# Performance work log

Measured on AMD Instinct MI355X. Metric: run time of the kernel, lower is better.

Reference implementation:

```python
import jax, jax.numpy as jnp
import numpy as np

N, E = 30000, 480000
IN_C, HID, HEADS = 128, 32, 8
HC = HID * HEADS  # 256
EPS = 1e-5
NEG_SLOPE = 0.2


def setup_inputs() -> dict:
    key = jax.random.key(0)
    ks = jax.random.split(key, 20)
    s = 0.05
    return {
        "x": jax.random.normal(ks[0], (N, IN_C), jnp.float32),
        "edge_index": jax.random.randint(ks[1], (2, E), 0, N, jnp.int32),
        "W1": jax.random.normal(ks[2], (IN_C, HC), jnp.float32) * s,
        "a1_src": jax.random.normal(ks[3], (HEADS, HID), jnp.float32) * s,
        "a1_dst": jax.random.normal(ks[4], (HEADS, HID), jnp.float32) * s,
        "b1": jnp.zeros((HC,), jnp.float32),
        "g1": jnp.ones((HC,), jnp.float32),
        "be1": jnp.zeros((HC,), jnp.float32),
        "W2": jax.random.normal(ks[5], (HC, HC), jnp.float32) * s,
        "a2_src": jax.random.normal(ks[6], (HEADS, HID), jnp.float32) * s,
        "a2_dst": jax.random.normal(ks[7], (HEADS, HID), jnp.float32) * s,
        "b2": jnp.zeros((HC,), jnp.float32),
        "g2": jnp.ones((HC,), jnp.float32),
        "be2": jnp.zeros((HC,), jnp.float32),
        "lW1": jax.random.normal(ks[8], (HC, HID), jnp.float32) * s,
        "lb1": jnp.zeros((HID,), jnp.float32),
        "lW2": jax.random.normal(ks[9], (HID, 1), jnp.float32) * s,
        "lb2": jnp.zeros((1,), jnp.float32),
    }


def gat_layer(x, src, dst, W, a_s, a_d, b):
    # x: [N, Fin] -> h: [N, H, C]
    h = (x @ W).reshape(N, HEADS, HID)
    al_s = jnp.sum(h * a_s, axis=-1)  # [N, H]
    al_d = jnp.sum(h * a_d, axis=-1)  # [N, H]
    e = jax.nn.leaky_relu(al_s[src] + al_d[dst], NEG_SLOPE)  # [E', H]
    # segment softmax over incoming edges of each destination node
    e = e - jax.ops.segment_max(e, dst, num_segments=N)[dst]
    ex = jnp.exp(e)
    alpha = ex / jax.ops.segment_sum(ex, dst, num_segments=N)[dst]
    msg = h[src] * alpha[:, :, None]  # [E', H, C]
    out = jax.ops.segment_sum(msg, dst, num_segments=N)  # [N, H, C]
    return out.reshape(N, HC) + b


def batchnorm(x, g, b):
    m = jnp.mean(x, axis=0)
    v = jnp.var(x, axis=0)
    return (x - m) * jax.lax.rsqrt(v + EPS) * g + b


def reference(x, edge_index, W1, a1_src, a1_dst, b1, g1, be1,
              W2, a2_src, a2_dst, b2, g2, be2, lW1, lb1, lW2, lb2):
    # add self-loops (PyG GATConv default)
    loop = jnp.arange(N, dtype=edge_index.dtype)
    src = jnp.concatenate([edge_index[0], loop])
    dst = jnp.concatenate([edge_index[1], loop])

    h = jax.nn.elu(gat_layer(x, src, dst, W1, a1_src, a1_dst, b1))
    h = batchnorm(h, g1, be1)
    h = jax.nn.elu(gat_layer(h, src, dst, W2, a2_src, a2_dst, b2))
    h = batchnorm(h, g2, be2)
    h = jax.nn.elu(h @ lW1 + lb1)
    return h @ lW2 + lb2
```

## Files before the change

### kernel.cpp

```cpp
#include <hip/hip_runtime.h>
#include <math.h>

#define N_NODES 30000
#define E_EDGES 480000
#define EP (E_EDGES + N_NODES)
#define IN_CH 128
#define HID 32
#define HEADS 8
#define HC 256
#define BN_EPS 1e-5f
#define NEG_SLOPE 0.2f
#define SCAN_NB ((N_NODES + 1023) / 1024)
#define PART_SLOTS 64

typedef __attribute__((ext_vector_type(8))) short bf16x8;
typedef __attribute__((ext_vector_type(4))) float f32x4;

__device__ __forceinline__ float elu_f(float x) { return x > 0.f ? x : __expf(x) - 1.f; }
__device__ __forceinline__ float lrelu_f(float x) { return x >= 0.f ? x : NEG_SLOPE * x; }
__device__ __forceinline__ float bf2f(unsigned short u) {
    return __uint_as_float(((unsigned)u) << 16);
}
__device__ __forceinline__ unsigned short f2bf(float f) {
    unsigned u = __float_as_uint(f);
    return (unsigned short)((u + 0x7fffu + ((u >> 16) & 1u)) >> 16);
}

__global__ void wt_all_kernel(const float* __restrict__ W1, const float* __restrict__ W2,
                              const float* __restrict__ lW1,
                              unsigned short* __restrict__ wt1,
                              unsigned short* __restrict__ wt2,
                              unsigned short* __restrict__ wtm) {
    int i = blockIdx.x * 256 + threadIdx.x;
    if (i < IN_CH * HC) {
        int k = i >> 8, n = i & 255;
        wt1[(size_t)n * IN_CH + k] = f2bf(W1[i]);
    } else if (i < IN_CH * HC + HC * HC) {
        int j = i - IN_CH * HC;
        int k = j >> 8, n = j & 255;
        wt2[(size_t)n * HC + k] = f2bf(W2[j]);
    } else if (i < IN_CH * HC + HC * HC + HC * HID) {
        int j = i - IN_CH * HC - HC * HC;
        int k = j >> 5, n = j & 31;
        wtm[(size_t)n * HC + k] = f2bf(lW1[j]);
    }
}

__global__ __launch_bounds__(256) void gemm_mfma(const float* __restrict__ A32,
                                                 const unsigned short* __restrict__ Abf,
                                                 const unsigned short* __restrict__ Bt,
                                                 unsigned short* __restrict__ C,
                                                 float* __restrict__ al_s,
                                                 float* __restrict__ al_d,
                                                 const float* __restrict__ a_src,
                                                 const float* __restrict__ a_dst,
                                                 int M, int K,
                                                 const float* __restrict__ sc,
                                                 const float* __restrict__ sh) {
    __shared__ __align__(16) unsigned short As[64][40];
    __shared__ __align__(16) unsigned short Bs[256][40];
    int tid = threadIdx.x;
    int wave = tid >> 6, lane = tid & 63;
    int m = lane & 15, q = lane >> 4;
    int row0 = blockIdx.x * 64;
    f32x4 acc[4][4];
#pragma unroll
    for (int i = 0; i < 4; ++i)
#pragma unroll
        for (int j = 0; j < 4; ++j) acc[i][j] = (f32x4){0.f, 0.f, 0.f, 0.f};
    int ar = tid >> 2, aseg = tid & 3;
    for (int k0 = 0; k0 < K; k0 += 32) {
        float4 v0 = make_float4(0.f, 0.f, 0.f, 0.f), v1 = v0;
        int gr = row0 + ar;
        int c0 = k0 + aseg * 8;
        if (gr < M) {
            if (A32) {
                const float* ap = A32 + (size_t)gr * K + c0;
                v0 = *(const float4*)ap;
                v1 = *(const float4*)(ap + 4);
            } else {
                uint4 raw = *(const uint4*)(Abf + (size_t)gr * K + c0);
                v0.x = bf2f((unsigned short)raw.x); v0.y = bf2f((unsigned short)(raw.x >> 16));
                v0.z = bf2f((unsigned short)raw.y); v0.w = bf2f((unsigned short)(raw.y >> 16));
                v1.x = bf2f((unsigned short)raw.z); v1.y = bf2f((unsigned short)(raw.z >> 16));
                v1.z = bf2f((unsigned short)raw.w); v1.w = bf2f((unsigned short)(raw.w >> 16));
            }
        }
        if (sc) {
            float4 s0 = *(const float4*)(sc + c0), s1 = *(const float4*)(sc + c0 + 4);
            float4 t0 = *(const float4*)(sh + c0), t1 = *(const float4*)(sh + c0 + 4);
            v0.x = v0.x * s0.x + t0.x; v0.y = v0.y * s0.y + t0.y;
            v0.z = v0.z * s0.z + t0.z; v0.w = v0.w * s0.w + t0.w;
            v1.x = v1.x * s1.x + t1.x; v1.y = v1.y * s1.y + t1.y;
            v1.z = v1.z * s1.z + t1.z; v1.w = v1.w * s1.w + t1.w;
        }
        bf16x8 av;
        av[0] = (short)f2bf(v0.x); av[1] = (short)f2bf(v0.y);
        av[2] = (short)f2bf(v0.z); av[3] = (short)f2bf(v0.w);
        av[4] = (short)f2bf(v1.x); av[5] = (short)f2bf(v1.y);
        av[6] = (short)f2bf(v1.z); av[7] = (short)f2bf(v1.w);
        *(bf16x8*)(&As[ar][aseg * 8]) = av;
        const unsigned short* bp = Bt + (size_t)tid * K + k0;
#pragma unroll
        for (int sg = 0; sg < 4; ++sg)
            *(uint4*)(&Bs[tid][sg * 8]) = *(const uint4*)(bp + sg * 8);
        __syncthreads();
        bf16x8 a0 = *(const bf16x8*)(&As[m][q * 8]);
        bf16x8 a1 = *(const bf16x8*)(&As[16 + m][q * 8]);
        bf16x8 a2 = *(const bf16x8*)(&As[32 + m][q * 8]);
        bf16x8 a3 = *(const bf16x8*)(&As[48 + m][q * 8]);
#pragma unroll
        for (int ni = 0; ni < 4; ++ni) {
            bf16x8 b = *(const bf16x8*)(&Bs[(wave * 4 + ni) * 16 + m][q * 8]);
            acc[0][ni] = __builtin_amdgcn_mfma_f32_16x16x32_bf16(a0, b, acc[0][ni], 0, 0, 0);
            acc[1][ni] = __builtin_amdgcn_mfma_f32_16x16x32_bf16(a1, b, acc[1][ni], 0, 0, 0);
            acc[2][ni] = __builtin_amdgcn_mfma_f32_16x16x32_bf16(a2, b, acc[2][ni], 0, 0, 0);
            acc[3][ni] = __builtin_amdgcn_mfma_f32_16x16x32_bf16(a3, b, acc[3][ni], 0, 0, 0);
        }
        __syncthreads();
    }
    int col0 = wave * 64;
    float asv[4], adv[4];
#pragma unroll
    for (int ni = 0; ni < 4; ++ni) {
        asv[ni] = a_src[col0 + ni * 16 + m];
        adv[ni] = a_dst[col0 + ni * 16 + m];
    }
#pragma unroll
    for (int mi = 0; mi < 4; ++mi) {
#pragma unroll
        for (int r = 0; r < 4; ++r) {
            int grow = row0 + mi * 16 + q * 4 + r;
            bool gv = grow < M;
            if (gv) {
#pragma unroll
                for (int ni = 0; ni < 4; ++ni)
                    C[(size_t)grow * HC + col0 + ni * 16 + m] = f2bf(acc[mi][ni][r]);
            }
            float ps0 = acc[mi][0][r] * asv[0] + acc[mi][1][r] * asv[1];
            float pd0 = acc[mi][0][r] * adv[0] + acc[mi][1][r] * adv[1];
            float ps1 = acc[mi][2][r] * asv[2] + acc[mi][3][r] * asv[3];
            float pd1 = acc[mi][2][r] * adv[2] + acc[mi][3][r] * adv[3];
            ps0 += __shfl_xor(ps0, 1); pd0 += __shfl_xor(pd0, 1);
            ps1 += __shfl_xor(ps1, 1); pd1 += __shfl_xor(pd1, 1);
            ps0 += __shfl_xor(ps0, 2); pd0 += __shfl_xor(pd0, 2);
            ps1 += __shfl_xor(ps1, 2); pd1 += __shfl_xor(pd1, 2);
            ps0 += __shfl_xor(ps0, 4); pd0 += __shfl_xor(pd0, 4);
            ps1 += __shfl_xor(ps1, 4); pd1 += __shfl_xor(pd1, 4);
            ps0 += __shfl_xor(ps0, 8); pd0 += __shfl_xor(pd0, 8);
            ps1 += __shfl_xor(ps1, 8); pd1 += __shfl_xor(pd1, 8);
            if (gv) {
                if (m == 0) {
                    al_s[grow * HEADS + 2 * wave] = ps0;
                    al_d[grow * HEADS + 2 * wave] = pd0;
                } else if (m == 1) {
                    al_s[grow * HEADS + 2 * wave + 1] = ps1;
                    al_d[grow * HEADS + 2 * wave + 1] = pd1;
                }
            }
        }
    }
}

__global__ void deg_kernel(const int* __restrict__ ei, int* __restrict__ deg,
                           float* __restrict__ part) {
    int e = blockIdx.x * blockDim.x + threadIdx.x;
    if (e < 2 * PART_SLOTS * 512) part[e] = 0.f;
    if (e >= EP) return;
    int d = (e < E_EDGES) ? ei[E_EDGES + e] : e - E_EDGES;
    atomicAdd(deg + d, 1);
}

__global__ __launch_bounds__(1024) void scan_blk(const int* __restrict__ deg,
                                                 int* __restrict__ rs,
                                                 int* __restrict__ bsum) {
    __shared__ int sh[1024];
    int t = threadIdx.x;
    int i = blockIdx.x * 1024 + t;
    int v = (i < N_NODES) ? deg[i] : 0;
    sh[t] = v;
    __syncthreads();
    for (int off = 1; off < 1024; off <<= 1) {
        int tv = (t >= off) ? sh[t - off] : 0;
        __syncthreads();
        sh[t] += tv;
        __syncthreads();
    }
    if (i < N_NODES) rs[i] = sh[t] - v;
    if (t == 1023) bsum[blockIdx.x] = sh[1023];
}

__global__ __launch_bounds__(1024) void scan_add(int* __restrict__ rs,
                                                 int* __restrict__ cursor,
                                                 const int* __restrict__ bsum) {
    __shared__ int sh_off, sh_tot;
    int t = threadIdx.x;
    if (t < 64) {
        int v = (t < SCAN_NB) ? bsum[t] : 0;
        int pre = (t < (int)blockIdx.x) ? v : 0;
        int tot = v;
#pragma unroll
        for (int off = 1; off < 64; off <<= 1) {
            tot += __shfl_xor(tot, off);
            pre += __shfl_xor(pre, off);
        }
        if (t == 0) { sh_off = pre; sh_tot = tot; }
    }
    __syncthreads();
    int i = blockIdx.x * 1024 + t;
    if (i < N_NODES) {
        int v = rs[i] + sh_off;
        rs[i] = v;
        cursor[i] = v;
    } else if (i == N_NODES) {
        rs[N_NODES] = sh_tot;
    }
}

__global__ void scatter_kernel(const int* __restrict__ ei, int* __restrict__ cursor,
                               int* __restrict__ csr_src) {
    int e = blockIdx.x * blockDim.x + threadIdx.x;
    if (e >= EP) return;
    int s, d;
    if (e < E_EDGES) { s = ei[e]; d = ei[E_EDGES + e]; } else { s = d = e - E_EDGES; }
    int pos = atomicAdd(cursor + d, 1);
    csr_src[pos] = s;
}

__global__ __launch_bounds__(256) void attn_kernel(const uint4* __restrict__ h8,
                                                   const float* __restrict__ al_s,
                                                   const float* __restrict__ al_d,
                                                   const int* __restrict__ row_start,
                                                   const int* __restrict__ csr_src,
                                                   const float4* __restrict__ bias4,
                                                   uint4* __restrict__ out8,
                                                   float* __restrict__ part) {
    __shared__ float lds_s[4][256];
    __shared__ float lds_q[4][256];
    int wave = threadIdx.x >> 6;
    int d = blockIdx.x * 4 + wave;
    int lane = threadIdx.x & 63;
    int hh = lane & 7, eo = lane >> 3;
    int g = lane >> 5, c = lane & 31;
    int hl = c >> 2;
    int beg = row_start[d], end = row_start[d + 1];
    float ad = al_d[d * HEADS + hh];
    float ssum = 0.f;
    float acc[8];
#pragma unroll
    for (int t = 0; t < 8; ++t) acc[t] = 0.f;

#define PAIR_BODY(p)                                                      \
    {                                                                     \
        int e0 = 2 * (p) + g;                                             \
        int sj = __shfl(sreg, e0 * 8);                                    \
        float aj = __shfl(ex, e0 * 8 + hl);                               \
        uint4 v = h8[(size_t)sj * 32 + c];                                \
        acc[0] += aj * bf2f((unsigned short)v.x);                         \
        acc[1] += aj * bf2f((unsigned short)(v.x >> 16));                 \
        acc[2] += aj * bf2f((unsigned short)v.y);                         \
        acc[3] += aj * bf2f((unsigned short)(v.y >> 16));                 \
        acc[4] += aj * bf2f((unsigned short)v.z);                         \
        acc[5] += aj * bf2f((unsigned short)(v.z >> 16));                 \
        acc[6] += aj * bf2f((unsigned short)v.w);                         \
        acc[7] += aj * bf2f((unsigned short)(v.w >> 16));                 \
    }

    for (int i = beg; i < end; i += 8) {
        int chunk = end - i;
        if (chunk > 8) chunk = 8;
        int sreg = 0;
        float ex = 0.f;
        if (eo < chunk) {
            sreg = csr_src[i + eo];
            ex = __expf(lrelu_f(al_s[sreg * HEADS + hh] + ad));
        }
        ssum += ex;
        if (chunk == 8) {
#pragma unroll
            for (int p = 0; p < 4; ++p) PAIR_BODY(p);
        } else {
            int np = (chunk + 1) >> 1;
            for (int p = 0; p < np; ++p) PAIR_BODY(p);
        }
    }
#undef PAIR_BODY

#pragma unroll
    for (int t = 0; t < 8; ++t) acc[t] += __shfl_xor(acc[t], 32);
    ssum += __shfl_xor(ssum, 8);
    ssum += __shfl_xor(ssum, 16);
    ssum += __shfl_xor(ssum, 32);
    float inv = 1.f / __shfl(ssum, hl);

    float4 b0 = bias4[c * 2], b1 = bias4[c * 2 + 1];
    float o0 = elu_f(acc[0] * inv + b0.x);
    float o1 = elu_f(acc[1] * inv + b0.y);
    float o2 = elu_f(acc[2] * inv + b0.z);
    float o3 = elu_f(acc[3] * inv + b0.w);
    float o4 = elu_f(acc[4] * inv + b1.x);
    float o5 = elu_f(acc[5] * inv + b1.y);
    float o6 = elu_f(acc[6] * inv + b1.z);
    float o7 = elu_f(acc[7] * inv + b1.w);

    if (g == 0) {
        uint4 ov;
        ov.x = (unsigned)f2bf(o0) | ((unsigned)f2bf(o1) << 16);
        ov.y = (unsigned)f2bf(o2) | ((unsigned)f2bf(o3) << 16);
        ov.z = (unsigned)f2bf(o4) | ((unsigned)f2bf(o5) << 16);
        ov.w = (unsigned)f2bf(o6) | ((unsigned)f2bf(o7) << 16);
        out8[(size_t)d * 32 + c] = ov;
        int cb = c * 8;
        lds_s[wave][cb + 0] = o0; lds_q[wave][cb + 0] = o0 * o0;
        lds_s[wave][cb + 1] = o1; lds_q[wave][cb + 1] = o1 * o1;
        lds_s[wave][cb + 2] = o2; lds_q[wave][cb + 2] = o2 * o2;
        lds_s[wave][cb + 3] = o3; lds_q[wave][cb + 3] = o3 * o3;
        lds_s[wave][cb + 4] = o4; lds_q[wave][cb + 4] = o4 * o4;
        lds_s[wave][cb + 5] = o5; lds_q[wave][cb + 5] = o5 * o5;
        lds_s[wave][cb + 6] = o6; lds_q[wave][cb + 6] = o6 * o6;
        lds_s[wave][cb + 7] = o7; lds_q[wave][cb + 7] = o7 * o7;
    }
    __syncthreads();
    int ch = threadIdx.x;
    float s = lds_s[0][ch] + lds_s[1][ch] + lds_s[2][ch] + lds_s[3][ch];
    float q = lds_q[0][ch] + lds_q[1][ch] + lds_q[2][ch] + lds_q[3][ch];
    float* pb = part + (size_t)(blockIdx.x & (PART_SLOTS - 1)) * 512;
    atomicAdd(pb + ch, s);
    atomicAdd(pb + 256 + ch, q);
}

__global__ void bn_fin_kernel(const float* __restrict__ part,
                              const float* __restrict__ g, const float* __restrict__ be,
                              float* __restrict__ scale, float* __restrict__ shift) {
    int c = threadIdx.x;
    float s = 0.f, q = 0.f;
#pragma unroll
    for (int b = 0; b < PART_SLOTS; ++b) {
        s += part[(size_t)b * 512 + c];
        q += part[(size_t)b * 512 + 256 + c];
    }
    float m = s / (float)N_NODES;
    float var = q / (float)N_NODES - m * m;
    float istd = rsqrtf(var + BN_EPS);
    float sc = istd * g[c];
    scale[c] = sc;
    shift[c] = be[c] - m * sc;
}

__global__ __launch_bounds__(256) void mlp_mfma(const unsigned short* __restrict__ in,
                                                const float* __restrict__ sc,
                                                const float* __restrict__ sh,
                                                const unsigned short* __restrict__ Wt,
                                                const float* __restrict__ lb1,
                                                const float* __restrict__ lW2,
                                                const float* __restrict__ lb2,
                                                float* __restrict__ out) {
    int tid = threadIdx.x;
    int wave = tid >> 6, lane = tid & 63;
    int m = lane & 15, q = lane >> 4;
    int rbase = blockIdx.x * 64 + wave * 16;
    int arow = rbase + m;
    bool valid = arow < N_NODES;
    const unsigned short* ap = in + (size_t)arow * HC;
    f32x4 acc0 = (f32x4){0.f, 0.f, 0.f, 0.f}, acc1 = acc0;
#pragma unroll
    for (int k0 = 0; k0 < HC; k0 += 32) {
        int c0 = k0 + q * 8;
        bf16x8 b0 = *(const bf16x8*)(Wt + (size_t)m * HC + c0);
        bf16x8 b1 = *(const bf16x8*)(Wt + (size_t)(m + 16) * HC + c0);
        bf16x8 a = (bf16x8){0, 0, 0, 0, 0, 0, 0, 0};
        if (valid) {
            uint4 raw = *(const uint4*)(ap + c0);
            float v0 = bf2f((unsigned short)raw.x), v1 = bf2f((unsigned short)(raw.x >> 16));
            float v2 = bf2f((unsigned short)raw.y), v3 = bf2f((unsigned short)(raw.y >> 16));
            float v4 = bf2f((unsigned short)raw.z), v5 = bf2f((unsigned short)(raw.z >> 16));
            float v6 = bf2f((unsigned short)raw.w), v7 = bf2f((unsigned short)(raw.w >> 16));
            float4 s0 = *(const float4*)(sc + c0), s1 = *(const float4*)(sc + c0 + 4);
            float4 t0 = *(const float4*)(sh + c0), t1 = *(const float4*)(sh + c0 + 4);
            a[0] = (short)f2bf(v0 * s0.x + t0.x);
            a[1] = (short)f2bf(v1 * s0.y + t0.y);
            a[2] = (short)f2bf(v2 * s0.z + t0.z);
            a[3] = (short)f2bf(v3 * s0.w + t0.w);
            a[4] = (short)f2bf(v4 * s1.x + t1.x);
            a[5] = (short)f2bf(v5 * s1.y + t1.y);
            a[6] = (short)f2bf(v6 * s1.z + t1.z);
            a[7] = (short)f2bf(v7 * s1.w + t1.w);
        }
        acc0 = __builtin_amdgcn_mfma_f32_16x16x32_bf16(a, b0, acc0, 0, 0, 0);
        acc1 = __builtin_amdgcn_mfma_f32_16x16x32_bf16(a, b1, acc1, 0, 0, 0);
    }
    float w2a = lW2[m], w2b = lW2[m + 16];
    float ba = lb1[m], bb = lb1[m + 16];
#pragma unroll
    for (int r = 0; r < 4; ++r) {
        float v = elu_f(acc0[r] + ba) * w2a + elu_f(acc1[r] + bb) * w2b;
        v += __shfl_xor(v, 1);
        v += __shfl_xor(v, 2);
        v += __shfl_xor(v, 4);
        v += __shfl_xor(v, 8);
        int orow = rbase + q * 4 + r;
        if (m == 0 && orow < N_NODES) out[orow] = v + lb2[0];
    }
}

extern "C" void kernel_launch(void* const* d_in, const int* in_sizes, int n_in,
                              void* d_out, int out_size, void* d_ws, size_t ws_size,
                              hipStream_t stream) {
    const float* x   = (const float*)d_in[0];
    const int*   ei  = (const int*)d_in[1];
    const float* W1  = (const float*)d_in[2];
    const float* a1s = (const float*)d_in[3];
    const float* a1d = (const float*)d_in[4];
    const float* b1  = (const float*)d_in[5];
    const float* g1  = (const float*)d_in[6];
    const float* be1 = (const float*)d_in[7];
    const float* W2  = (const float*)d_in[8];
    const float* a2s = (const float*)d_in[9];
    const float* a2d = (const float*)d_in[10];
    const float* b2  = (const float*)d_in[11];
    const float* g2  = (const float*)d_in[12];
    const float* be2 = (const float*)d_in[13];
    const float* lW1 = (const float*)d_in[14];
    const float* lb1 = (const float*)d_in[15];
    const float* lW2 = (const float*)d_in[16];
    const float* lb2 = (const float*)d_in[17];
    float* out = (float*)d_out;

    char* p = (char*)d_ws;
    auto alloc = [&](size_t bytes) {
        char* r = p;
        p += (bytes + 255) & ~(size_t)255;
        return r;
    };
    unsigned short* h_bf  = (unsigned short*)alloc((size_t)N_NODES * HC * 2);
    unsigned short* o_bf  = (unsigned short*)alloc((size_t)N_NODES * HC * 2);
    unsigned short* wt1   = (unsigned short*)alloc((size_t)IN_CH * HC * 2);
    unsigned short* wt2   = (unsigned short*)alloc((size_t)HC * HC * 2);
    unsigned short* wtm   = (unsigned short*)alloc((size_t)HC * HID * 2);
    float* f_als  = (float*)alloc((size_t)N_NODES * HEADS * 4);
    float* f_ald  = (float*)alloc((size_t)N_NODES * HEADS * 4);
    int*   i_deg  = (int*)alloc((size_t)N_NODES * 4);
    int*   i_rs   = (int*)alloc((size_t)(N_NODES + 1) * 4);
    int*   i_cur  = (int*)alloc((size_t)N_NODES * 4);
    int*   i_src  = (int*)alloc((size_t)EP * 4);
    int*   i_bsum = (int*)alloc((size_t)(SCAN_NB + 1) * 4);
    float* f_part = (float*)alloc((size_t)2 * PART_SLOTS * 512 * 4);
    float* f_sc1  = (float*)alloc(HC * 4);
    float* f_sh1  = (float*)alloc(HC * 4);
    float* f_sc2  = (float*)alloc(HC * 4);
    float* f_sh2  = (float*)alloc(HC * 4);

    int eb = (EP + 255) / 256;

    hipMemsetAsync(i_deg, 0, (size_t)N_NODES * 4, stream);
    deg_kernel<<<eb, 256, 0, stream>>>(ei, i_deg, f_part);
    scan_blk<<<SCAN_NB, 1024, 0, stream>>>(i_deg, i_rs, i_bsum);
    scan_add<<<SCAN_NB, 1024, 0, stream>>>(i_rs, i_cur, i_bsum);
    scatter_kernel<<<eb, 256, 0, stream>>>(ei, i_cur, i_src);

    int wtot = IN_CH * HC + HC * HC + HC * HID;
    wt_all_kernel<<<(wtot + 255) / 256, 256, 0, stream>>>(W1, W2, lW1, wt1, wt2, wtm);

    int gblocks = (N_NODES + 63) / 64;

    auto run_layer = [&](const float* A32, const unsigned short* Abf, int K,
                         const unsigned short* wt, const float* in_sc, const float* in_sh,
                         const float* as_, const float* ad_, const float* bias,
                         const float* gam, const float* bet, float* part,
                         float* out_sc, float* out_sh) {
        gemm_mfma<<<gblocks, 256, 0, stream>>>(A32, Abf, wt, h_bf, f_als, f_ald, as_, ad_,
                                               N_NODES, K, in_sc, in_sh);
        attn_kernel<<<N_NODES / 4, 256, 0, stream>>>((const uint4*)h_bf, f_als, f_ald,
                                                     i_rs, i_src, (const float4*)bias,
                                                     (uint4*)o_bf, part);
        bn_fin_kernel<<<1, 256, 0, stream>>>(part, gam, bet, out_sc, out_sh);
    };

    run_layer(x, nullptr, IN_CH, wt1, nullptr, nullptr, a1s, a1d, b1, g1, be1,
              f_part, f_sc1, f_sh1);
    run_layer(nullptr, o_bf, HC, wt2, f_sc1, f_sh1, a2s, a2d, b2, g2, be2,
              f_part + (size_t)PART_SLOTS * 512, f_sc2, f_sh2);

    mlp_mfma<<<gblocks, 256, 0, stream>>>(o_bf, f_sc2, f_sh2, wtm, lb1, lW2, lb2, out);
}
```

Before: 295.6 us.

## Fold BN finalize into consumers, enlarge GEMM tile, batch attention gathers

Removes the separate single-block BN finalize kernels; each GEMM and MLP block now reduces the partial sums itself into shared scale/shift. The GEMM block grows to 512 threads covering 128 rows, so each B tile staged in shared memory is reused by twice as many rows. The attention loop handles 16 edges per iteration and issues all eight row gathers before the FMAs, to keep more memory loads in flight. The cost is that every block repeats the 64-slot partial reduction, and the larger unrolled loop uses more registers.

```diff
diff --git a/kernel.cpp b/kernel.cpp
--- a/kernel.cpp
+++ b/kernel.cpp
@@ -46,7 +46,7 @@
     }
 }
 
-__global__ __launch_bounds__(256) void gemm_mfma(const float* __restrict__ A32,
+__global__ __launch_bounds__(512) void gemm_mfma(const float* __restrict__ A32,
                                                  const unsigned short* __restrict__ Abf,
                                                  const unsigned short* __restrict__ Bt,
                                                  unsigned short* __restrict__ C,
@@ -55,20 +55,44 @@
                                                  const float* __restrict__ a_src,
                                                  const float* __restrict__ a_dst,
                                                  int M, int K,
-                                                 const float* __restrict__ sc,
-                                                 const float* __restrict__ sh) {
-    __shared__ __align__(16) unsigned short As[64][40];
+                                                 const float* __restrict__ part,
+                                                 const float* __restrict__ gam,
+                                                 const float* __restrict__ bet) {
+    __shared__ __align__(16) unsigned short As[128][40];
     __shared__ __align__(16) unsigned short Bs[256][40];
+    __shared__ float scs[HC], shs[HC];
     int tid = threadIdx.x;
     int wave = tid >> 6, lane = tid & 63;
     int m = lane & 15, q = lane >> 4;
-    int row0 = blockIdx.x * 64;
+    int wr = (wave >> 2) * 64;
+    int hp = wave & 3;
+    int col0 = hp * 64;
+    int row0 = blockIdx.x * 128;
+    bool haveBN = (part != nullptr);
+    if (haveBN && tid < HC) {
+        int c = tid;
+        float s = 0.f, qq = 0.f;
+#pragma unroll
+        for (int b = 0; b < PART_SLOTS; ++b) {
+            s += part[(size_t)b * 512 + c];
+            qq += part[(size_t)b * 512 + 256 + c];
+        }
+        float mn = s / (float)N_NODES;
+        float var = qq / (float)N_NODES - mn * mn;
+        float istd = rsqrtf(var + BN_EPS);
+        float sc = istd * gam[c];
+        scs[c] = sc;
+        shs[c] = bet[c] - mn * sc;
+    }
+    __syncthreads();
+
     f32x4 acc[4][4];
 #pragma unroll
     for (int i = 0; i < 4; ++i)
 #pragma unroll
         for (int j = 0; j < 4; ++j) acc[i][j] = (f32x4){0.f, 0.f, 0.f, 0.f};
     int ar = tid >> 2, aseg = tid & 3;
+    int br = tid >> 1, bseg = tid & 1;
     for (int k0 = 0; k0 < K; k0 += 32) {
         float4 v0 = make_float4(0.f, 0.f, 0.f, 0.f), v1 = v0;
         int gr = row0 + ar;
@@ -86,9 +110,9 @@
                 v1.z = bf2f((unsigned short)raw.w); v1.w = bf2f((unsigned short)(raw.w >> 16));
             }
         }
-        if (sc) {
-            float4 s0 = *(const float4*)(sc + c0), s1 = *(const float4*)(sc + c0 + 4);
-            float4 t0 = *(const float4*)(sh + c0), t1 = *(const float4*)(sh + c0 + 4);
+        if (haveBN) {
+            float4 s0 = *(const float4*)(scs + c0), s1 = *(const float4*)(scs + c0 + 4);
+            float4 t0 = *(const float4*)(shs + c0), t1 = *(const float4*)(shs + c0 + 4);
             v0.x = v0.x * s0.x + t0.x; v0.y = v0.y * s0.y + t0.y;
             v0.z = v0.z * s0.z + t0.z; v0.w = v0.w * s0.w + t0.w;
             v1.x = v1.x * s1.x + t1.x; v1.y = v1.y * s1.y + t1.y;
@@ -100,18 +124,17 @@
         av[4] = (short)f2bf(v1.x); av[5] = (short)f2bf(v1.y);
         av[6] = (short)f2bf(v1.z); av[7] = (short)f2bf(v1.w);
         *(bf16x8*)(&As[ar][aseg * 8]) = av;
-        const unsigned short* bp = Bt + (size_t)tid * K + k0;
-#pragma unroll
-        for (int sg = 0; sg < 4; ++sg)
-            *(uint4*)(&Bs[tid][sg * 8]) = *(const uint4*)(bp + sg * 8);
+        const unsigned short* bp = Bt + (size_t)br * K + k0 + bseg * 16;
+        *(uint4*)(&Bs[br][bseg * 16]) = *(const uint4*)bp;
+        *(uint4*)(&Bs[br][bseg * 16 + 8]) = *(const uint4*)(bp + 8);
         __syncthreads();
-        bf16x8 a0 = *(const bf16x8*)(&As[m][q * 8]);
-        bf16x8 a1 = *(const bf16x8*)(&As[16 + m][q * 8]);
-        bf16x8 a2 = *(const bf16x8*)(&As[32 + m][q * 8]);
-        bf16x8 a3 = *(const bf16x8*)(&As[48 + m][q * 8]);
+        bf16x8 a0 = *(const bf16x8*)(&As[wr + m][q * 8]);
+        bf16x8 a1 = *(const bf16x8*)(&As[wr + 16 + m][q * 8]);
+        bf16x8 a2 = *(const bf16x8*)(&As[wr + 32 + m][q * 8]);
+        bf16x8 a3 = *(const bf16x8*)(&As[wr + 48 + m][q * 8]);
 #pragma unroll
         for (int ni = 0; ni < 4; ++ni) {
-            bf16x8 b = *(const bf16x8*)(&Bs[(wave * 4 + ni) * 16 + m][q * 8]);
+            bf16x8 b = *(const bf16x8*)(&Bs[col0 + ni * 16 + m][q * 8]);
             acc[0][ni] = __builtin_amdgcn_mfma_f32_16x16x32_bf16(a0, b, acc[0][ni], 0, 0, 0);
             acc[1][ni] = __builtin_amdgcn_mfma_f32_16x16x32_bf16(a1, b, acc[1][ni], 0, 0, 0);
             acc[2][ni] = __builtin_amdgcn_mfma_f32_16x16x32_bf16(a2, b, acc[2][ni], 0, 0, 0);
@@ -119,7 +142,6 @@
         }
         __syncthreads();
     }
-    int col0 = wave * 64;
     float asv[4], adv[4];
 #pragma unroll
     for (int ni = 0; ni < 4; ++ni) {
@@ -130,7 +152,7 @@
     for (int mi = 0; mi < 4; ++mi) {
 #pragma unroll
         for (int r = 0; r < 4; ++r) {
-            int grow = row0 + mi * 16 + q * 4 + r;
+            int grow = row0 + wr + mi * 16 + q * 4 + r;
             bool gv = grow < M;
             if (gv) {
 #pragma unroll
@@ -151,11 +173,11 @@
             ps1 += __shfl_xor(ps1, 8); pd1 += __shfl_xor(pd1, 8);
             if (gv) {
                 if (m == 0) {
-                    al_s[grow * HEADS + 2 * wave] = ps0;
-                    al_d[grow * HEADS + 2 * wave] = pd0;
+                    al_s[grow * HEADS + 2 * hp] = ps0;
+                    al_d[grow * HEADS + 2 * hp] = pd0;
                 } else if (m == 1) {
-                    al_s[grow * HEADS + 2 * wave + 1] = ps1;
-                    al_d[grow * HEADS + 2 * wave + 1] = pd1;
+                    al_s[grow * HEADS + 2 * hp + 1] = ps1;
+                    al_d[grow * HEADS + 2 * hp + 1] = pd1;
                 }
             }
         }
@@ -250,12 +272,8 @@
 #pragma unroll
     for (int t = 0; t < 8; ++t) acc[t] = 0.f;
 
-#define PAIR_BODY(p)                                                      \
+#define FMA8(v, aj)                                                       \
     {                                                                     \
-        int e0 = 2 * (p) + g;                                             \
-        int sj = __shfl(sreg, e0 * 8);                                    \
-        float aj = __shfl(ex, e0 * 8 + hl);                               \
-        uint4 v = h8[(size_t)sj * 32 + c];                                \
         acc[0] += aj * bf2f((unsigned short)v.x);                         \
         acc[1] += aj * bf2f((unsigned short)(v.x >> 16));                 \
         acc[2] += aj * bf2f((unsigned short)v.y);                         \
@@ -265,26 +283,49 @@
         acc[6] += aj * bf2f((unsigned short)v.w);                         \
         acc[7] += aj * bf2f((unsigned short)(v.w >> 16));                 \
     }
-
-    for (int i = beg; i < end; i += 8) {
-        int chunk = end - i;
-        if (chunk > 8) chunk = 8;
-        int sreg = 0;
-        float ex = 0.f;
-        if (eo < chunk) {
-            sreg = csr_src[i + eo];
-            ex = __expf(lrelu_f(al_s[sreg * HEADS + hh] + ad));
-        }
-        ssum += ex;
-        if (chunk == 8) {
-#pragma unroll
-            for (int p = 0; p < 4; ++p) PAIR_BODY(p);
+#define PRE(k, SR, EX, p)                                                 \
+    int sj##k = __shfl(SR, (2 * (p) + g) * 8);                            \
+    float aj##k = __shfl(EX, (2 * (p) + g) * 8 + hl);                     \
+    uint4 w##k = h8[(size_t)sj##k * 32 + c];
+#define PAIR(SR, EX, p)                                                   \
+    {                                                                     \
+        PRE(t, SR, EX, p)                                                 \
+        FMA8(w##t, aj##t)                                                 \
+    }
+
+    for (int i = beg; i < end; i += 16) {
+        int rem = end - i;
+        int cntA = rem > 8 ? 8 : rem;
+        int cntB = rem > 8 ? (rem > 16 ? 8 : rem - 8) : 0;
+        int sregA = 0, sregB = 0;
+        float exA = 0.f, exB = 0.f;
+        if (eo < cntA) {
+            sregA = csr_src[i + eo];
+            exA = __expf(lrelu_f(al_s[sregA * HEADS + hh] + ad));
+        }
+        if (eo < cntB) {
+            sregB = csr_src[i + 8 + eo];
+            exB = __expf(lrelu_f(al_s[sregB * HEADS + hh] + ad));
+        }
+        ssum += exA;
+        ssum += exB;
+        if (rem >= 16) {
+            PRE(0, sregA, exA, 0) PRE(1, sregA, exA, 1)
+            PRE(2, sregA, exA, 2) PRE(3, sregA, exA, 3)
+            PRE(4, sregB, exB, 0) PRE(5, sregB, exB, 1)
+            PRE(6, sregB, exB, 2) PRE(7, sregB, exB, 3)
+            FMA8(w0, aj0) FMA8(w1, aj1) FMA8(w2, aj2) FMA8(w3, aj3)
+            FMA8(w4, aj4) FMA8(w5, aj5) FMA8(w6, aj6) FMA8(w7, aj7)
         } else {
-            int np = (chunk + 1) >> 1;
-            for (int p = 0; p < np; ++p) PAIR_BODY(p);
-        }
-    }
-#undef PAIR_BODY
+            int npA = (cntA + 1) >> 1;
+            for (int p = 0; p < npA; ++p) PAIR(sregA, exA, p);
+            int npB = (cntB + 1) >> 1;
+            for (int p = 0; p < npB; ++p) PAIR(sregB, exB, p);
+        }
+    }
+#undef PAIR
+#undef PRE
+#undef FMA8
 
 #pragma unroll
     for (int t = 0; t < 8; ++t) acc[t] += __shfl_xor(acc[t], 32);
@@ -329,33 +370,33 @@
     atomicAdd(pb + 256 + ch, q);
 }
 
-__global__ void bn_fin_kernel(const float* __restrict__ part,
-                              const float* __restrict__ g, const float* __restrict__ be,
-                              float* __restrict__ scale, float* __restrict__ shift) {
-    int c = threadIdx.x;
-    float s = 0.f, q = 0.f;
-#pragma unroll
-    for (int b = 0; b < PART_SLOTS; ++b) {
-        s += part[(size_t)b * 512 + c];
-        q += part[(size_t)b * 512 + 256 + c];
-    }
-    float m = s / (float)N_NODES;
-    float var = q / (float)N_NODES - m * m;
-    float istd = rsqrtf(var + BN_EPS);
-    float sc = istd * g[c];
-    scale[c] = sc;
-    shift[c] = be[c] - m * sc;
-}
-
 __global__ __launch_bounds__(256) void mlp_mfma(const unsigned short* __restrict__ in,
-                                                const float* __restrict__ sc,
-                                                const float* __restrict__ sh,
+                                                const float* __restrict__ part,
+                                                const float* __restrict__ gam,
+                                                const float* __restrict__ bet,
                                                 const unsigned short* __restrict__ Wt,
                                                 const float* __restrict__ lb1,
                                                 const float* __restrict__ lW2,
                                                 const float* __restrict__ lb2,
                                                 float* __restrict__ out) {
+    __shared__ float scs[HC], shs[HC];
     int tid = threadIdx.x;
+    {
+        int c = tid;
+        float s = 0.f, qq = 0.f;
+#pragma unroll
+        for (int b = 0; b < PART_SLOTS; ++b) {
+            s += part[(size_t)b * 512 + c];
+            qq += part[(size_t)b * 512 + 256 + c];
+        }
+        float mn = s / (float)N_NODES;
+        float var = qq / (float)N_NODES - mn * mn;
+        float istd = rsqrtf(var + BN_EPS);
+        float sc = istd * gam[c];
+        scs[c] = sc;
+        shs[c] = bet[c] - mn * sc;
+    }
+    __syncthreads();
     int wave = tid >> 6, lane = tid & 63;
     int m = lane & 15, q = lane >> 4;
     int rbase = blockIdx.x * 64 + wave * 16;
@@ -375,8 +416,8 @@
             float v2 = bf2f((unsigned short)raw.y), v3 = bf2f((unsigned short)(raw.y >> 16));
             float v4 = bf2f((unsigned short)raw.z), v5 = bf2f((unsigned short)(raw.z >> 16));
             float v6 = bf2f((unsigned short)raw.w), v7 = bf2f((unsigned short)(raw.w >> 16));
-            float4 s0 = *(const float4*)(sc + c0), s1 = *(const float4*)(sc + c0 + 4);
-            float4 t0 = *(const float4*)(sh + c0), t1 = *(const float4*)(sh + c0 + 4);
+            float4 s0 = *(const float4*)(scs + c0), s1 = *(const float4*)(scs + c0 + 4);
+            float4 t0 = *(const float4*)(shs + c0), t1 = *(const float4*)(shs + c0 + 4);
             a[0] = (short)f2bf(v0 * s0.x + t0.x);
             a[1] = (short)f2bf(v1 * s0.y + t0.y);
             a[2] = (short)f2bf(v2 * s0.z + t0.z);
@@ -445,10 +486,6 @@
     int*   i_src  = (int*)alloc((size_t)EP * 4);
     int*   i_bsum = (int*)alloc((size_t)(SCAN_NB + 1) * 4);
     float* f_part = (float*)alloc((size_t)2 * PART_SLOTS * 512 * 4);
-    float* f_sc1  = (float*)alloc(HC * 4);
-    float* f_sh1  = (float*)alloc(HC * 4);
-    float* f_sc2  = (float*)alloc(HC * 4);
-    float* f_sh2  = (float*)alloc(HC * 4);
 
     int eb = (EP + 255) / 256;
 
@@ -461,25 +498,20 @@
     int wtot = IN_CH * HC + HC * HC + HC * HID;
     wt_all_kernel<<<(wtot + 255) / 256, 256, 0, stream>>>(W1, W2, lW1, wt1, wt2, wtm);
 
-    int gblocks = (N_NODES + 63) / 64;
-
-    auto run_layer = [&](const float* A32, const unsigned short* Abf, int K,
-                         const unsigned short* wt, const float* in_sc, const float* in_sh,
-                         const float* as_, const float* ad_, const float* bias,
-                         const float* gam, const float* bet, float* part,
-                         float* out_sc, float* out_sh) {
-        gemm_mfma<<<gblocks, 256, 0, stream>>>(A32, Abf, wt, h_bf, f_als, f_ald, as_, ad_,
-                                               N_NODES, K, in_sc, in_sh);
-        attn_kernel<<<N_NODES / 4, 256, 0, stream>>>((const uint4*)h_bf, f_als, f_ald,
-                                                     i_rs, i_src, (const float4*)bias,
-                                                     (uint4*)o_bf, part);
-        bn_fin_kernel<<<1, 256, 0, stream>>>(part, gam, bet, out_sc, out_sh);
-    };
-
-    run_layer(x, nullptr, IN_CH, wt1, nullptr, nullptr, a1s, a1d, b1, g1, be1,
-              f_part, f_sc1, f_sh1);
-    run_layer(nullptr, o_bf, HC, wt2, f_sc1, f_sh1, a2s, a2d, b2, g2, be2,
-              f_part + (size_t)PART_SLOTS * 512, f_sc2, f_sh2);
-
-    mlp_mfma<<<gblocks, 256, 0, stream>>>(o_bf, f_sc2, f_sh2, wtm, lb1, lW2, lb2, out);
-}
+    int gblocks = (N_NODES + 127) / 128;
+    float* part1 = f_part;
+    float* part2 = f_part + (size_t)PART_SLOTS * 512;
+
+    gemm_mfma<<<gblocks, 512, 0, stream>>>(x, nullptr, wt1, h_bf, f_als, f_ald, a1s, a1d,
+                                           N_NODES, IN_CH, nullptr, nullptr, nullptr);
+    attn_kernel<<<N_NODES / 4, 256, 0, stream>>>((const uint4*)h_bf, f_als, f_ald,
+                                                 i_rs, i_src, (const float4*)b1,
+                                                 (uint4*)o_bf, part1);
+    gemm_mfma<<<gblocks, 512, 0, stream>>>(nullptr, o_bf, wt2, h_bf, f_als, f_ald, a2s, a2d,
+                                           N_NODES, HC, part1, g1, be1);
+    attn_kernel<<<N_NODES / 4, 256, 0, stream>>>((const uint4*)h_bf, f_als, f_ald,
+                                                 i_rs, i_src, (const float4*)b2,
+                                                 (uint4*)o_bf, part2);
+    mlp_mfma<<<(N_NODES + 63) / 64, 256, 0, stream>>>(o_bf, part2, g2, be2, wtm,
+                                                      lb1, lW2, lb2, out);
+}
```

Result: no change. 295.3 us (-0.1%).

## Fold batchnorm into next-layer weights and use async LDS loads in GEMM

Applied to the files above, without the earlier changes.

Batchnorm scale and shift are folded into the following weight matrices and a per-column bias (fold2/fold3 kernels), so the GEMM and MLP read plain bf16 activations without per-element affine transforms. The GEMM now stages tiles with global_load_lds into a swizzled LDS layout and uses 128-row tiles with 512 threads. The input x is converted to bf16 by a separate pass. Folding the scale into the weights before bf16 rounding changes rounding behaviour slightly. The GEMM has no row bounds check on its loads and instead relies on padded input buffers (M_PAD).

```diff
diff --git a/kernel.cpp b/kernel.cpp
--- a/kernel.cpp
+++ b/kernel.cpp
@@ -12,6 +12,7 @@
 #define NEG_SLOPE 0.2f
 #define SCAN_NB ((N_NODES + 1023) / 1024)
 #define PART_SLOTS 64
+#define M_PAD 30080
 
 typedef __attribute__((ext_vector_type(8))) short bf16x8;
 typedef __attribute__((ext_vector_type(4))) float f32x4;
@@ -26,92 +27,148 @@
     return (unsigned short)((u + 0x7fffu + ((u >> 16) & 1u)) >> 16);
 }
 
-__global__ void wt_all_kernel(const float* __restrict__ W1, const float* __restrict__ W2,
-                              const float* __restrict__ lW1,
-                              unsigned short* __restrict__ wt1,
-                              unsigned short* __restrict__ wt2,
-                              unsigned short* __restrict__ wtm) {
+#define GLD16(gp, lp)                                                      \
+    __builtin_amdgcn_global_load_lds(                                      \
+        (const __attribute__((address_space(1))) unsigned int*)(gp),       \
+        (__attribute__((address_space(3))) unsigned int*)(lp), 16, 0, 0)
+
+__global__ void wt_all_kernel(const float* __restrict__ W1,
+                              unsigned short* __restrict__ wt1) {
     int i = blockIdx.x * 256 + threadIdx.x;
     if (i < IN_CH * HC) {
         int k = i >> 8, n = i & 255;
         wt1[(size_t)n * IN_CH + k] = f2bf(W1[i]);
-    } else if (i < IN_CH * HC + HC * HC) {
-        int j = i - IN_CH * HC;
-        int k = j >> 8, n = j & 255;
-        wt2[(size_t)n * HC + k] = f2bf(W2[j]);
-    } else if (i < IN_CH * HC + HC * HC + HC * HID) {
-        int j = i - IN_CH * HC - HC * HC;
-        int k = j >> 5, n = j & 31;
-        wtm[(size_t)n * HC + k] = f2bf(lW1[j]);
-    }
-}
-
-__global__ __launch_bounds__(256) void gemm_mfma(const float* __restrict__ A32,
-                                                 const unsigned short* __restrict__ Abf,
+    }
+}
+
+__global__ void xconv_kernel(const float* __restrict__ x, unsigned short* __restrict__ xbf) {
+    int i = blockIdx.x * 256 + threadIdx.x;
+    if (i * 8 >= N_NODES * IN_CH) return;
+    const float4* xp = (const float4*)(x + (size_t)i * 8);
+    float4 v0 = xp[0], v1 = xp[1];
+    ushort4 o0, o1;
+    o0.x = f2bf(v0.x); o0.y = f2bf(v0.y); o0.z = f2bf(v0.z); o0.w = f2bf(v0.w);
+    o1.x = f2bf(v1.x); o1.y = f2bf(v1.y); o1.z = f2bf(v1.z); o1.w = f2bf(v1.w);
+    ushort4* op = (ushort4*)(xbf + (size_t)i * 8);
+    op[0] = o0; op[1] = o1;
+}
+
+__global__ __launch_bounds__(256) void fold2_kernel(const float* __restrict__ W2,
+                                                    const float* __restrict__ part,
+                                                    const float* __restrict__ g,
+                                                    const float* __restrict__ be,
+                                                    unsigned short* __restrict__ wt2p,
+                                                    float* __restrict__ cb2) {
+    __shared__ float red[256];
+    int n = blockIdx.x, k = threadIdx.x;
+    float s = 0.f, qq = 0.f;
+#pragma unroll
+    for (int b = 0; b < PART_SLOTS; ++b) {
+        s += part[(size_t)b * 512 + k];
+        qq += part[(size_t)b * 512 + 256 + k];
+    }
+    float mn = s / (float)N_NODES;
+    float var = qq / (float)N_NODES - mn * mn;
+    float istd = rsqrtf(var + BN_EPS);
+    float sck = istd * g[k];
+    float shk = be[k] - mn * sck;
+    float w = W2[(size_t)k * HC + n];
+    wt2p[(size_t)n * HC + k] = f2bf(w * sck);
+    red[k] = shk * w;
+    __syncthreads();
+    for (int off = 128; off > 0; off >>= 1) {
+        if (k < off) red[k] += red[k + off];
+        __syncthreads();
+    }
+    if (k == 0) cb2[n] = red[0];
+}
+
+__global__ __launch_bounds__(256) void fold3_kernel(const float* __restrict__ lW1,
+                                                    const float* __restrict__ part,
+                                                    const float* __restrict__ g,
+                                                    const float* __restrict__ be,
+                                                    const float* __restrict__ lb1,
+                                                    unsigned short* __restrict__ wtmp,
+                                                    float* __restrict__ lb1p) {
+    __shared__ float red[256];
+    int n = blockIdx.x, k = threadIdx.x;
+    float s = 0.f, qq = 0.f;
+#pragma unroll
+    for (int b = 0; b < PART_SLOTS; ++b) {
+        s += part[(size_t)b * 512 + k];
+        qq += part[(size_t)b * 512 + 256 + k];
+    }
+    float mn = s / (float)N_NODES;
+    float var = qq / (float)N_NODES - mn * mn;
+    float istd = rsqrtf(var + BN_EPS);
+    float sck = istd * g[k];
+    float shk = be[k] - mn * sck;
+    float w = lW1[(size_t)k * HID + n];
+    wtmp[(size_t)n * HC + k] = f2bf(w * sck);
+    red[k] = shk * w;
+    __syncthreads();
+    for (int off = 128; off > 0; off >>= 1) {
+        if (k < off) red[k] += red[k + off];
+        __syncthreads();
+    }
+    if (k == 0) lb1p[n] = lb1[n] + red[0];
+}
+
+__global__ __launch_bounds__(512) void gemm_mfma(const unsigned short* __restrict__ Abf,
                                                  const unsigned short* __restrict__ Bt,
+                                                 const float* __restrict__ cb,
                                                  unsigned short* __restrict__ C,
                                                  float* __restrict__ al_s,
                                                  float* __restrict__ al_d,
                                                  const float* __restrict__ a_src,
                                                  const float* __restrict__ a_dst,
-                                                 int M, int K,
-                                                 const float* __restrict__ sc,
-                                                 const float* __restrict__ sh) {
-    __shared__ __align__(16) unsigned short As[64][40];
-    __shared__ __align__(16) unsigned short Bs[256][40];
+                                                 int M, int K) {
+    __shared__ __align__(16) unsigned short As[128 * 32];
+    __shared__ __align__(16) unsigned short Bs[256 * 32];
     int tid = threadIdx.x;
     int wave = tid >> 6, lane = tid & 63;
     int m = lane & 15, q = lane >> 4;
-    int row0 = blockIdx.x * 64;
+    int wr = (wave >> 2) * 64;
+    int hp = wave & 3;
+    int col0 = hp * 64;
+    int row0 = blockIdx.x * 128;
+
+    int sA = wave * 64 + lane;
+    int rA = sA >> 2, scA = sA & 3;
+    int ccA = scA ^ (rA & 3) ^ ((rA >> 2) & 3);
+    const unsigned short* aSrc = Abf + (size_t)(row0 + rA) * K + ccA * 8;
+    unsigned short* aDst = As + wave * 512;
+    int sB0 = wave * 128 + lane;
+    int rB0 = sB0 >> 2, scB0 = sB0 & 3;
+    int ccB0 = scB0 ^ (rB0 & 3) ^ ((rB0 >> 2) & 3);
+    const unsigned short* bSrc0 = Bt + (size_t)rB0 * K + ccB0 * 8;
+    unsigned short* bDst0 = Bs + wave * 1024;
+    int sB1 = sB0 + 64;
+    int rB1 = sB1 >> 2, scB1 = sB1 & 3;
+    int ccB1 = scB1 ^ (rB1 & 3) ^ ((rB1 >> 2) & 3);
+    const unsigned short* bSrc1 = Bt + (size_t)rB1 * K + ccB1 * 8;
+    unsigned short* bDst1 = Bs + wave * 1024 + 512;
+
+    int ccr8 = (q ^ (m & 3) ^ ((m >> 2) & 3)) * 8;
+
     f32x4 acc[4][4];
 #pragma unroll
     for (int i = 0; i < 4; ++i)
 #pragma unroll
         for (int j = 0; j < 4; ++j) acc[i][j] = (f32x4){0.f, 0.f, 0.f, 0.f};
-    int ar = tid >> 2, aseg = tid & 3;
+
     for (int k0 = 0; k0 < K; k0 += 32) {
-        float4 v0 = make_float4(0.f, 0.f, 0.f, 0.f), v1 = v0;
-        int gr = row0 + ar;
-        int c0 = k0 + aseg * 8;
-        if (gr < M) {
-            if (A32) {
-                const float* ap = A32 + (size_t)gr * K + c0;
-                v0 = *(const float4*)ap;
-                v1 = *(const float4*)(ap + 4);
-            } else {
-                uint4 raw = *(const uint4*)(Abf + (size_t)gr * K + c0);
-                v0.x = bf2f((unsigned short)raw.x); v0.y = bf2f((unsigned short)(raw.x >> 16));
-                v0.z = bf2f((unsigned short)raw.y); v0.w = bf2f((unsigned short)(raw.y >> 16));
-                v1.x = bf2f((unsigned short)raw.z); v1.y = bf2f((unsigned short)(raw.z >> 16));
-                v1.z = bf2f((unsigned short)raw.w); v1.w = bf2f((unsigned short)(raw.w >> 16));
-            }
-        }
-        if (sc) {
-            float4 s0 = *(const float4*)(sc + c0), s1 = *(const float4*)(sc + c0 + 4);
-            float4 t0 = *(const float4*)(sh + c0), t1 = *(const float4*)(sh + c0 + 4);
-            v0.x = v0.x * s0.x + t0.x; v0.y = v0.y * s0.y + t0.y;
-            v0.z = v0.z * s0.z + t0.z; v0.w = v0.w * s0.w + t0.w;
-            v1.x = v1.x * s1.x + t1.x; v1.y = v1.y * s1.y + t1.y;
-            v1.z = v1.z * s1.z + t1.z; v1.w = v1.w * s1.w + t1.w;
-        }
-        bf16x8 av;
-        av[0] = (short)f2bf(v0.x); av[1] = (short)f2bf(v0.y);
-        av[2] = (short)f2bf(v0.z); av[3] = (short)f2bf(v0.w);
-        av[4] = (short)f2bf(v1.x); av[5] = (short)f2bf(v1.y);
-        av[6] = (short)f2bf(v1.z); av[7] = (short)f2bf(v1.w);
-        *(bf16x8*)(&As[ar][aseg * 8]) = av;
-        const unsigned short* bp = Bt + (size_t)tid * K + k0;
-#pragma unroll
-        for (int sg = 0; sg < 4; ++sg)
-            *(uint4*)(&Bs[tid][sg * 8]) = *(const uint4*)(bp + sg * 8);
+        GLD16(aSrc + k0, aDst);
+        GLD16(bSrc0 + k0, bDst0);
+        GLD16(bSrc1 + k0, bDst1);
         __syncthreads();
-        bf16x8 a0 = *(const bf16x8*)(&As[m][q * 8]);
-        bf16x8 a1 = *(const bf16x8*)(&As[16 + m][q * 8]);
-        bf16x8 a2 = *(const bf16x8*)(&As[32 + m][q * 8]);
-        bf16x8 a3 = *(const bf16x8*)(&As[48 + m][q * 8]);
+        bf16x8 a0 = *(const bf16x8*)(As + (wr + m) * 32 + ccr8);
+        bf16x8 a1 = *(const bf16x8*)(As + (wr + 16 + m) * 32 + ccr8);
+        bf16x8 a2 = *(const bf16x8*)(As + (wr + 32 + m) * 32 + ccr8);
+        bf16x8 a3 = *(const bf16x8*)(As + (wr + 48 + m) * 32 + ccr8);
 #pragma unroll
         for (int ni = 0; ni < 4; ++ni) {
-            bf16x8 b = *(const bf16x8*)(&Bs[(wave * 4 + ni) * 16 + m][q * 8]);
+            bf16x8 b = *(const bf16x8*)(Bs + (col0 + ni * 16 + m) * 32 + ccr8);
             acc[0][ni] = __builtin_amdgcn_mfma_f32_16x16x32_bf16(a0, b, acc[0][ni], 0, 0, 0);
             acc[1][ni] = __builtin_amdgcn_mfma_f32_16x16x32_bf16(a1, b, acc[1][ni], 0, 0, 0);
             acc[2][ni] = __builtin_amdgcn_mfma_f32_16x16x32_bf16(a2, b, acc[2][ni], 0, 0, 0);
@@ -119,7 +176,16 @@
         }
         __syncthreads();
     }
-    int col0 = wave * 64;
+    float cbv[4];
+#pragma unroll
+    for (int ni = 0; ni < 4; ++ni) cbv[ni] = cb[col0 + ni * 16 + m];
+#pragma unroll
+    for (int mi = 0; mi < 4; ++mi)
+#pragma unroll
+        for (int ni = 0; ni < 4; ++ni)
+#pragma unroll
+            for (int r = 0; r < 4; ++r) acc[mi][ni][r] += cbv[ni];
+
     float asv[4], adv[4];
 #pragma unroll
     for (int ni = 0; ni < 4; ++ni) {
@@ -130,7 +196,7 @@
     for (int mi = 0; mi < 4; ++mi) {
 #pragma unroll
         for (int r = 0; r < 4; ++r) {
-            int grow = row0 + mi * 16 + q * 4 + r;
+            int grow = row0 + wr + mi * 16 + q * 4 + r;
             bool gv = grow < M;
             if (gv) {
 #pragma unroll
@@ -151,11 +217,11 @@
             ps1 += __shfl_xor(ps1, 8); pd1 += __shfl_xor(pd1, 8);
             if (gv) {
                 if (m == 0) {
-                    al_s[grow * HEADS + 2 * wave] = ps0;
-                    al_d[grow * HEADS + 2 * wave] = pd0;
+                    al_s[grow * HEADS + 2 * hp] = ps0;
+                    al_d[grow * HEADS + 2 * hp] = pd0;
                 } else if (m == 1) {
-                    al_s[grow * HEADS + 2 * wave + 1] = ps1;
-                    al_d[grow * HEADS + 2 * wave + 1] = pd1;
+                    al_s[grow * HEADS + 2 * hp + 1] = ps1;
+                    al_d[grow * HEADS + 2 * hp + 1] = pd1;
                 }
             }
         }
@@ -165,7 +231,7 @@
 __global__ void deg_kernel(const int* __restrict__ ei, int* __restrict__ deg,
                            float* __restrict__ part) {
     int e = blockIdx.x * blockDim.x + threadIdx.x;
-    if (e < 2 * PART_SLOTS * 512) part[e] = 0.f;
+    if (e < 2 * PART_SLOTS * 512 + 256) part[e] = 0.f;
     if (e >= EP) return;
     int d = (e < E_EDGES) ? ei[E_EDGES + e] : e - E_EDGES;
     atomicAdd(deg + d, 1);
@@ -329,29 +395,9 @@
     atomicAdd(pb + 256 + ch, q);
 }
 
-__global__ void bn_fin_kernel(const float* __restrict__ part,
-                              const float* __restrict__ g, const float* __restrict__ be,
-                              float* __restrict__ scale, float* __restrict__ shift) {
-    int c = threadIdx.x;
-    float s = 0.f, q = 0.f;
-#pragma unroll
-    for (int b = 0; b < PART_SLOTS; ++b) {
-        s += part[(size_t)b * 512 + c];
-        q += part[(size_t)b * 512 + 256 + c];
-    }
-    float m = s / (float)N_NODES;
-    float var = q / (float)N_NODES - m * m;
-    float istd = rsqrtf(var + BN_EPS);
-    float sc = istd * g[c];
-    scale[c] = sc;
-    shift[c] = be[c] - m * sc;
-}
-
 __global__ __launch_bounds__(256) void mlp_mfma(const unsigned short* __restrict__ in,
-                                                const float* __restrict__ sc,
-                                                const float* __restrict__ sh,
                                                 const unsigned short* __restrict__ Wt,
-                                                const float* __restrict__ lb1,
+                                                const float* __restrict__ lb1p,
                                                 const float* __restrict__ lW2,
                                                 const float* __restrict__ lb2,
                                                 float* __restrict__ out) {
@@ -369,28 +415,12 @@
         bf16x8 b0 = *(const bf16x8*)(Wt + (size_t)m * HC + c0);
         bf16x8 b1 = *(const bf16x8*)(Wt + (size_t)(m + 16) * HC + c0);
         bf16x8 a = (bf16x8){0, 0, 0, 0, 0, 0, 0, 0};
-        if (valid) {
-            uint4 raw = *(const uint4*)(ap + c0);
-            float v0 = bf2f((unsigned short)raw.x), v1 = bf2f((unsigned short)(raw.x >> 16));
-            float v2 = bf2f((unsigned short)raw.y), v3 = bf2f((unsigned short)(raw.y >> 16));
-            float v4 = bf2f((unsigned short)raw.z), v5 = bf2f((unsigned short)(raw.z >> 16));
-            float v6 = bf2f((unsigned short)raw.w), v7 = bf2f((unsigned short)(raw.w >> 16));
-            float4 s0 = *(const float4*)(sc + c0), s1 = *(const float4*)(sc + c0 + 4);
-            float4 t0 = *(const float4*)(sh + c0), t1 = *(const float4*)(sh + c0 + 4);
-            a[0] = (short)f2bf(v0 * s0.x + t0.x);
-            a[1] = (short)f2bf(v1 * s0.y + t0.y);
-            a[2] = (short)f2bf(v2 * s0.z + t0.z);
-            a[3] = (short)f2bf(v3 * s0.w + t0.w);
-            a[4] = (short)f2bf(v4 * s1.x + t1.x);
-            a[5] = (short)f2bf(v5 * s1.y + t1.y);
-            a[6] = (short)f2bf(v6 * s1.z + t1.z);
-            a[7] = (short)f2bf(v7 * s1.w + t1.w);
-        }
+        if (valid) a = *(const bf16x8*)(ap + c0);
         acc0 = __builtin_amdgcn_mfma_f32_16x16x32_bf16(a, b0, acc0, 0, 0, 0);
         acc1 = __builtin_amdgcn_mfma_f32_16x16x32_bf16(a, b1, acc1, 0, 0, 0);
     }
     float w2a = lW2[m], w2b = lW2[m + 16];
-    float ba = lb1[m], bb = lb1[m + 16];
+    float ba = lb1p[m], bb = lb1p[m + 16];
 #pragma unroll
     for (int r = 0; r < 4; ++r) {
         float v = elu_f(acc0[r] + ba) * w2a + elu_f(acc1[r] + bb) * w2b;
@@ -432,11 +462,12 @@
         p += (bytes + 255) & ~(size_t)255;
         return r;
     };
+    unsigned short* x_bf  = (unsigned short*)alloc((size_t)M_PAD * IN_CH * 2);
     unsigned short* h_bf  = (unsigned short*)alloc((size_t)N_NODES * HC * 2);
-    unsigned short* o_bf  = (unsigned short*)alloc((size_t)N_NODES * HC * 2);
+    unsigned short* o_bf  = (unsigned short*)alloc((size_t)M_PAD * HC * 2);
     unsigned short* wt1   = (unsigned short*)alloc((size_t)IN_CH * HC * 2);
-    unsigned short* wt2   = (unsigned short*)alloc((size_t)HC * HC * 2);
-    unsigned short* wtm   = (unsigned short*)alloc((size_t)HC * HID * 2);
+    unsigned short* wt2p  = (unsigned short*)alloc((size_t)HC * HC * 2);
+    unsigned short* wtmp  = (unsigned short*)alloc((size_t)HC * HID * 2);
     float* f_als  = (float*)alloc((size_t)N_NODES * HEADS * 4);
     float* f_ald  = (float*)alloc((size_t)N_NODES * HEADS * 4);
     int*   i_deg  = (int*)alloc((size_t)N_NODES * 4);
@@ -444,11 +475,13 @@
     int*   i_cur  = (int*)alloc((size_t)N_NODES * 4);
     int*   i_src  = (int*)alloc((size_t)EP * 4);
     int*   i_bsum = (int*)alloc((size_t)(SCAN_NB + 1) * 4);
-    float* f_part = (float*)alloc((size_t)2 * PART_SLOTS * 512 * 4);
-    float* f_sc1  = (float*)alloc(HC * 4);
-    float* f_sh1  = (float*)alloc(HC * 4);
-    float* f_sc2  = (float*)alloc(HC * 4);
-    float* f_sh2  = (float*)alloc(HC * 4);
+    float* f_part = (float*)alloc(((size_t)2 * PART_SLOTS * 512 + 256) * 4);
+    float* f_cb2  = (float*)alloc(HC * 4);
+    float* f_lb1p = (float*)alloc(HID * 4);
+
+    float* part1 = f_part;
+    float* part2 = f_part + (size_t)PART_SLOTS * 512;
+    float* cb0   = f_part + (size_t)2 * PART_SLOTS * 512;
 
     int eb = (EP + 255) / 256;
 
@@ -458,28 +491,22 @@
     scan_add<<<SCAN_NB, 1024, 0, stream>>>(i_rs, i_cur, i_bsum);
     scatter_kernel<<<eb, 256, 0, stream>>>(ei, i_cur, i_src);
 
-    int wtot = IN_CH * HC + HC * HC + HC * HID;
-    wt_all_kernel<<<(wtot + 255) / 256, 256, 0, stream>>>(W1, W2, lW1, wt1, wt2, wtm);
-
-    int gblocks = (N_NODES + 63) / 64;
-
-    auto run_layer = [&](const float* A32, const unsigned short* Abf, int K,
-                         const unsigned short* wt, const float* in_sc, const float* in_sh,
-                         const float* as_, const float* ad_, const float* bias,
-                         const float* gam, const float* bet, float* part,
-                         float* out_sc, float* out_sh) {
-        gemm_mfma<<<gblocks, 256, 0, stream>>>(A32, Abf, wt, h_bf, f_als, f_ald, as_, ad_,
-                                               N_NODES, K, in_sc, in_sh);
-        attn_kernel<<<N_NODES / 4, 256, 0, stream>>>((const uint4*)h_bf, f_als, f_ald,
-                                                     i_rs, i_src, (const float4*)bias,
-                                                     (uint4*)o_bf, part);
-        bn_fin_kernel<<<1, 256, 0, stream>>>(part, gam, bet, out_sc, out_sh);
-    };
-
-    run_layer(x, nullptr, IN_CH, wt1, nullptr, nullptr, a1s, a1d, b1, g1, be1,
-              f_part, f_sc1, f_sh1);
-    run_layer(nullptr, o_bf, HC, wt2, f_sc1, f_sh1, a2s, a2d, b2, g2, be2,
-              f_part + (size_t)PART_SLOTS * 512, f_sc2, f_sh2);
-
-    mlp_mfma<<<gblocks, 256, 0, stream>>>(o_bf, f_sc2, f_sh2, wtm, lb1, lW2, lb2, out);
-}
+    wt_all_kernel<<<(IN_CH * HC + 255) / 256, 256, 0, stream>>>(W1, wt1);
+    xconv_kernel<<<(N_NODES * IN_CH / 8 + 255) / 256, 256, 0, stream>>>(x, x_bf);
+
+    int gblocks = (N_NODES + 127) / 128;
+
+    gemm_mfma<<<gblocks, 512, 0, stream>>>(x_bf, wt1, cb0, h_bf, f_als, f_ald, a1s, a1d,
+                                           N_NODES, IN_CH);
+    attn_kernel<<<N_NODES / 4, 256, 0, stream>>>((const uint4*)h_bf, f_als, f_ald,
+                                                 i_rs, i_src, (const float4*)b1,
+                                                 (uint4*)o_bf, part1);
+    fold2_kernel<<<HC, 256, 0, stream>>>(W2, part1, g1, be1, wt2p, f_cb2);
+    gemm_mfma<<<gblocks, 512, 0, stream>>>(o_bf, wt2p, f_cb2, h_bf, f_als, f_ald, a2s, a2d,
+                                           N_NODES, HC);
+    attn_kernel<<<N_NODES / 4, 256, 0, stream>>>((const uint4*)h_bf, f_als, f_ald,
+                                                 i_rs, i_src, (const float4*)b2,
+                                                 (uint4*)o_bf, part2);
+    fold3_kernel<<<HID, 256, 0, stream>>>(lW1, part2, g2, be2, lb1, wtmp, f_lb1p);
+    mlp_mfma<<<(N_NODES + 63) / 64, 256, 0, stream>>>(o_bf, wtmp, f_lb1p, lW2, lb2, out);
+}
```

Measured after the change: 296.0 us. No clear change (+0.1%).
